# Kernel tuning notes

Hardware: AMD Instinct MI355X
Metric: run time of the kernel (lower is better)

Reference implementation:

```python
import jax, jax.numpy as jnp
import numpy as np

EMBED_DIM = 256
NUM_HEADS = 8
HEAD_DIM = EMBED_DIM // NUM_HEADS
SCALE = HEAD_DIM ** (-0.5)
L, B = 2048, 2


def setup_inputs() -> dict:
    key = jax.random.key(0)
    ks = jax.random.split(key, 12)
    s = EMBED_DIM ** (-0.5)
    return {
        "query": jax.random.normal(ks[0], (L, B, EMBED_DIM), jnp.float32),
        "key_": jax.random.normal(ks[1], (L, B, EMBED_DIM), jnp.float32),
        "value": jax.random.normal(ks[2], (L, B, EMBED_DIM), jnp.float32),
        "Wq": jax.random.normal(ks[3], (EMBED_DIM, EMBED_DIM), jnp.float32) * s,
        "bq": jnp.zeros((EMBED_DIM,), jnp.float32),
        "Wk": jax.random.normal(ks[4], (EMBED_DIM, EMBED_DIM), jnp.float32) * s,
        "bk": jnp.zeros((EMBED_DIM,), jnp.float32),
        "Wv": jax.random.normal(ks[5], (EMBED_DIM, EMBED_DIM), jnp.float32) * s,
        "bv": jnp.zeros((EMBED_DIM,), jnp.float32),
        "Wp": jax.random.normal(ks[6], (EMBED_DIM, EMBED_DIM), jnp.float32) * s,
        "bp": jnp.zeros((EMBED_DIM,), jnp.float32),
    }


def reference(query, key_, value, Wq, bq, Wk, bk, Wv, bv, Wp, bp):
    # Inputs are seq-first: [L, B, E]. Dropout treated as eval (identity).
    Lq, Bq, E = query.shape
    q = (query @ Wq + bq).reshape(Lq, Bq, NUM_HEADS, HEAD_DIM)
    k = (key_ @ Wk + bk).reshape(key_.shape[0], Bq, NUM_HEADS, HEAD_DIM)
    v = (value @ Wv + bv).reshape(value.shape[0], Bq, NUM_HEADS, HEAD_DIM)
    # scores: [B, H, Lq, Lk]
    attn = jnp.einsum('qbhd,kbhd->bhqk', q, k) * SCALE
    attn = jax.nn.softmax(attn, axis=-1)
    out = jnp.einsum('bhqk,kbhd->qbhd', attn, v).reshape(Lq, Bq, E)
    return out @ Wp + bp
```

## Files before the change

### kernel.cpp

```cpp
#include <hip/hip_runtime.h>
#include <math.h>

#define L_SEQ 2048
#define BATCH 2
#define EMB   256
#define NH    8
#define HD    32
#define NROW  (L_SEQ * BATCH)
#define SCALE 0.17677669529663687f
#define LOG2E 1.4426950408889634f
#define SCLAMP 60.0f

typedef __attribute__((ext_vector_type(8))) short          short8;
typedef __attribute__((ext_vector_type(8))) unsigned short ushort8v;
typedef __attribute__((ext_vector_type(4))) unsigned short ushort4v;
typedef __attribute__((ext_vector_type(4))) float          floatx4;

__device__ __forceinline__ unsigned short f2b(float x) {
    unsigned int u = __float_as_uint(x);
    unsigned int r = u + 0x7FFFu + ((u >> 16) & 1u);
    return (unsigned short)(r >> 16);
}

__device__ __forceinline__ unsigned int pack2bf(float lo, float hi) {
    unsigned int ulo = __float_as_uint(lo);
    unsigned int uhi = __float_as_uint(hi);
    ulo += 0x7FFFu + ((ulo >> 16) & 1u);
    uhi += 0x7FFFu + ((uhi >> 16) & 1u);
    return __builtin_amdgcn_perm(uhi, ulo, 0x07060302);
}

__device__ __forceinline__ float b2f(unsigned short u) {
    return __uint_as_float(((unsigned int)u) << 16);
}

__device__ __forceinline__ float hw_exp2(float x) {
    return __builtin_amdgcn_exp2f(x);
}

__global__ __launch_bounds__(256) void wtrans_kernel(const float* __restrict__ Wq,
                                                     const float* __restrict__ Wk,
                                                     const float* __restrict__ Wv,
                                                     const float* __restrict__ Wp,
                                                     unsigned short* __restrict__ out) {
    __shared__ unsigned short T[64][65];
    const int wsel = blockIdx.z;
    const float* W = (wsel == 0) ? Wq : (wsel == 1) ? Wk : (wsel == 2) ? Wv : Wp;
    const float scale = (wsel == 0) ? (SCALE * LOG2E) : 1.0f;
    unsigned short* dst = out + (size_t)wsel * EMB * EMB;
    const int k0 = blockIdx.x * 64, n0 = blockIdx.y * 64;
    const int tid = threadIdx.x;

    #pragma unroll
    for (int i = 0; i < 4; ++i) {
        int idx = tid + 256 * i;
        int r = idx >> 4, c4 = (idx & 15) * 4;
        float4 f = *(const float4*)&W[(size_t)(k0 + r) * EMB + n0 + c4];
        T[r][c4 + 0] = f2b(f.x * scale);
        T[r][c4 + 1] = f2b(f.y * scale);
        T[r][c4 + 2] = f2b(f.z * scale);
        T[r][c4 + 3] = f2b(f.w * scale);
    }
    __syncthreads();
    #pragma unroll
    for (int i = 0; i < 4; ++i) {
        int idx = tid + 256 * i;
        int rn = idx >> 4, ck = (idx & 15) * 4;
        ushort4v p;
        #pragma unroll
        for (int j = 0; j < 4; ++j) p[j] = T[ck + j][rn];
        *(ushort4v*)&dst[(size_t)(n0 + rn) * EMB + k0 + ck] = p;
    }
}

__global__ __launch_bounds__(256) void qkv_proj(const float* __restrict__ Xq,
                                                const float* __restrict__ Xk,
                                                const float* __restrict__ Xv,
                                                const unsigned short* __restrict__ Wt,
                                                const float* __restrict__ bq,
                                                const float* __restrict__ bk,
                                                const float* __restrict__ bv,
                                                unsigned short* __restrict__ outq,
                                                unsigned short* __restrict__ outk,
                                                unsigned short* __restrict__ outvt) {
    __shared__ unsigned short Xs[64][136];
    __shared__ unsigned short Ws[64][136];
    const int z = blockIdx.z;
    const float* X    = (z == 0) ? Xq : (z == 1) ? Xk : Xv;
    const float* bias = (z == 0) ? bq : (z == 1) ? bk : bv;
    const float bscale = (z == 0) ? (SCALE * LOG2E) : 1.0f;
    const unsigned short* W = Wt + (size_t)z * EMB * EMB;

    const int row0 = blockIdx.x * 64;
    const int col0 = blockIdx.y * 64;
    const int tid  = threadIdx.x;
    const int w    = tid >> 6;
    const int lane = tid & 63;
    const int l16  = lane & 15;
    const int quad = lane >> 4;

    floatx4 acc[4];
    #pragma unroll
    for (int g = 0; g < 4; ++g) acc[g] = (floatx4){0.f, 0.f, 0.f, 0.f};

    #pragma unroll
    for (int kh = 0; kh < 2; ++kh) {
        if (kh) __syncthreads();
        #pragma unroll
        for (int i = 0; i < 4; ++i) {
            int idx = tid + 256 * i;
            int r = idx >> 4, c8 = (idx & 15) * 8;
            const float4* xp = (const float4*)&X[(size_t)(row0 + r) * EMB + kh * 128 + c8];
            float4 f0 = xp[0], f1 = xp[1];
            uint4 pk;
            pk.x = pack2bf(f0.x, f0.y); pk.y = pack2bf(f0.z, f0.w);
            pk.z = pack2bf(f1.x, f1.y); pk.w = pack2bf(f1.z, f1.w);
            *(uint4*)&Xs[r][c8] = pk;
            *(ushort8v*)&Ws[r][c8] =
                *(const ushort8v*)&W[(size_t)(col0 + r) * EMB + kh * 128 + c8];
        }
        __syncthreads();

        #pragma unroll
        for (int k = 0; k < 128; k += 32) {
            short8 a = *(const short8*)&Xs[w * 16 + l16][k + quad * 8];
            #pragma unroll
            for (int g = 0; g < 4; ++g) {
                short8 bf = *(const short8*)&Ws[g * 16 + l16][k + quad * 8];
                acc[g] = __builtin_amdgcn_mfma_f32_16x16x32_bf16(a, bf, acc[g], 0, 0, 0);
            }
        }
    }

    if (z == 2) {
        __syncthreads();
        #pragma unroll
        for (int g = 0; g < 4; ++g) {
            int n = g * 16 + l16;
            float bb = bias[col0 + n] * bscale;
            #pragma unroll
            for (int r = 0; r < 4; ++r)
                Xs[w * 16 + quad * 4 + r][n] = f2b(acc[g][r] + bb);
        }
        __syncthreads();
        #pragma unroll
        for (int i = 0; i < 2; ++i) {
            int idx = tid + 256 * i;
            int n = idx >> 3, sub = idx & 7;
            int bb2 = sub >> 2, lq = sub & 3;
            ushort8v p;
            #pragma unroll
            for (int j = 0; j < 8; ++j) p[j] = Xs[(lq * 8 + j) * 2 + bb2][n];
            int h = (col0 + n) >> 5, d = (col0 + n) & 31;
            size_t base = ((size_t)(bb2 * NH + h) * HD + d) * L_SEQ + (row0 >> 1) + lq * 8;
            *(ushort8v*)&outvt[base] = p;
        }
    } else {
        unsigned short* outp = z ? outk : outq;
        #pragma unroll
        for (int g = 0; g < 4; ++g) {
            int c = col0 + g * 16 + l16;
            float bb = bias[c] * bscale;
            #pragma unroll
            for (int r = 0; r < 4; ++r) {
                int rg = row0 + w * 16 + quad * 4 + r;
                int b = rg & 1, ll = rg >> 1;
                int h = c >> 5, d = c & 31;
                outp[(((size_t)(b * NH + h) * L_SEQ) + ll) * HD + d] = f2b(acc[g][r] + bb);
            }
        }
    }
}

__global__ __launch_bounds__(256) void attn_kernel(const unsigned short* __restrict__ Q,
                                                   const unsigned short* __restrict__ K,
                                                   const unsigned short* __restrict__ Vt,
                                                   unsigned short* __restrict__ Opart,
                                                   float* __restrict__ lpart) {
    __shared__ unsigned short Vs[2][32][136];
    __shared__ unsigned short Ps[4][16][136];

    const int tid  = threadIdx.x;
    const int w    = tid >> 6;
    const int lane = tid & 63;
    const int l16  = lane & 15;
    const int quad = lane >> 4;

    const int l0   = blockIdx.x * 64;
    const int h    = blockIdx.y;
    const int b    = blockIdx.z & 1;
    const int half = blockIdx.z >> 1;
    const int koff = half * (L_SEQ / 2);
    const size_t bh = (size_t)(b * NH + h);

    const unsigned short* Qg  = Q  + (bh * L_SEQ) * HD;
    const unsigned short* Kg  = K  + (bh * L_SEQ + koff) * HD;
    const unsigned short* Vtg = Vt + (bh * HD) * L_SEQ + koff;

    short8 qfrag = *(const short8*)&Qg[(size_t)(l0 + w * 16 + l16) * HD + quad * 8];

    float lacc = 0.0f;
    floatx4 o0 = {0.f, 0.f, 0.f, 0.f};
    floatx4 o1 = {0.f, 0.f, 0.f, 0.f};
    const floatx4 zero4 = {0.f, 0.f, 0.f, 0.f};

    const int vd = tid >> 3;
    const int vj = (tid & 7) * 8;

    short8 kf[8];
    #pragma unroll
    for (int g = 0; g < 8; ++g)
        kf[g] = *(const short8*)&Kg[(size_t)(g * 16 + l16) * HD + quad * 8];

    *(ushort8v*)&Vs[0][vd][vj]      = *(const ushort8v*)&Vtg[(size_t)vd * L_SEQ + vj];
    *(ushort8v*)&Vs[0][vd][64 + vj] = *(const ushort8v*)&Vtg[(size_t)vd * L_SEQ + 64 + vj];

    const int NT = (L_SEQ / 2) / 128;
    for (int kt = 0; kt < NT; ++kt) {
        __syncthreads();

        floatx4 s[8];
        #pragma unroll
        for (int g = 0; g < 8; ++g)
            s[g] = __builtin_amdgcn_mfma_f32_16x16x32_bf16(kf[g], qfrag, zero4, 0, 0, 0);

        ushort8v vn0, vn1;
        if (kt + 1 < NT) {
            #pragma unroll
            for (int g = 0; g < 8; ++g)
                kf[g] = *(const short8*)
                    &Kg[(size_t)((kt + 1) * 128 + g * 16 + l16) * HD + quad * 8];
            vn0 = *(const ushort8v*)&Vtg[(size_t)vd * L_SEQ + (kt + 1) * 128 + vj];
            vn1 = *(const ushort8v*)&Vtg[(size_t)vd * L_SEQ + (kt + 1) * 128 + 64 + vj];
        }

        #pragma unroll
        for (int g = 0; g < 8; ++g) {
            float p0 = hw_exp2(fminf(s[g][0], SCLAMP));
            float p1 = hw_exp2(fminf(s[g][1], SCLAMP));
            float p2 = hw_exp2(fminf(s[g][2], SCLAMP));
            float p3 = hw_exp2(fminf(s[g][3], SCLAMP));
            lacc += (p0 + p1) + (p2 + p3);
            uint2 pk;
            pk.x = pack2bf(p0, p1);
            pk.y = pack2bf(p2, p3);
            *(uint2*)&Ps[w][l16][g * 16 + quad * 4] = pk;
        }

        const unsigned short (*Vc)[136] = Vs[kt & 1];
        #pragma unroll
        for (int c = 0; c < 4; ++c) {
            short8 pf = *(const short8*)&Ps[w][l16][c * 32 + quad * 8];
            short8 va = *(const short8*)&Vc[l16][c * 32 + quad * 8];
            short8 vb = *(const short8*)&Vc[16 + l16][c * 32 + quad * 8];
            o0 = __builtin_amdgcn_mfma_f32_16x16x32_bf16(va, pf, o0, 0, 0, 0);
            o1 = __builtin_amdgcn_mfma_f32_16x16x32_bf16(vb, pf, o1, 0, 0, 0);
        }

        if (kt + 1 < NT) {
            *(ushort8v*)&Vs[(kt + 1) & 1][vd][vj]      = vn0;
            *(ushort8v*)&Vs[(kt + 1) & 1][vd][64 + vj] = vn1;
        }
    }

    lacc += __shfl_xor(lacc, 16);
    lacc += __shfl_xor(lacc, 32);

    int query = l0 + w * 16 + l16;
    if (lane < 16)
        lpart[(size_t)half * (BATCH * NH * L_SEQ) + bh * L_SEQ + query] = lacc;

    size_t base = (size_t)half * ((size_t)NROW * EMB) +
                  ((size_t)query * BATCH + b) * EMB + h * HD;
    uint2 e0, e1;
    e0.x = pack2bf(o0[0], o0[1]);
    e0.y = pack2bf(o0[2], o0[3]);
    e1.x = pack2bf(o1[0], o1[1]);
    e1.y = pack2bf(o1[2], o1[3]);
    *(uint2*)&Opart[base + quad * 4] = e0;
    *(uint2*)&Opart[base + 16 + quad * 4] = e1;
}

__global__ __launch_bounds__(256) void out_proj(const unsigned short* __restrict__ Opart,
                                                const float* __restrict__ lpart,
                                                const unsigned short* __restrict__ Wt,
                                                const float* __restrict__ bias,
                                                float* __restrict__ out) {
    __shared__ unsigned short Xs[32][264];
    __shared__ unsigned short Ws[32][264];
    const int row0 = blockIdx.x * 32;
    const int col0 = blockIdx.y * 32;
    const int tid  = threadIdx.x;
    const int w    = tid >> 6;
    const int rw   = (w & 1) * 16;
    const int cw   = (w >> 1) * 16;
    const int lane = tid & 63;
    const int l16  = lane & 15;
    const int quad = lane >> 4;

    const size_t OP = (size_t)NROW * EMB;
    const size_t LP = (size_t)BATCH * NH * L_SEQ;

    #pragma unroll
    for (int i = 0; i < 4; ++i) {
        int idx = tid + 256 * i;
        int r = idx >> 5, c8 = (idx & 31) * 8;
        int rg = row0 + r;
        int bb = rg & 1, q = rg >> 1, hh = c8 >> 5;
        size_t lidx = ((size_t)(bb * NH + hh)) * L_SEQ + q;
        float inv = __builtin_amdgcn_rcpf(lpart[lidx] + lpart[LP + lidx]);

        ushort8v u0 = *(const ushort8v*)&Opart[(size_t)rg * EMB + c8];
        ushort8v u1 = *(const ushort8v*)&Opart[OP + (size_t)rg * EMB + c8];
        uint4 pk;
        pk.x = pack2bf((b2f(u0[0]) + b2f(u1[0])) * inv, (b2f(u0[1]) + b2f(u1[1])) * inv);
        pk.y = pack2bf((b2f(u0[2]) + b2f(u1[2])) * inv, (b2f(u0[3]) + b2f(u1[3])) * inv);
        pk.z = pack2bf((b2f(u0[4]) + b2f(u1[4])) * inv, (b2f(u0[5]) + b2f(u1[5])) * inv);
        pk.w = pack2bf((b2f(u0[6]) + b2f(u1[6])) * inv, (b2f(u0[7]) + b2f(u1[7])) * inv);
        *(uint4*)&Xs[r][c8] = pk;

        *(ushort8v*)&Ws[r][c8] = *(const ushort8v*)&Wt[(size_t)(col0 + r) * EMB + c8];
    }
    __syncthreads();

    floatx4 acc = {0.f, 0.f, 0.f, 0.f};
    #pragma unroll
    for (int k = 0; k < EMB; k += 32) {
        short8 a  = *(const short8*)&Xs[rw + l16][k + quad * 8];
        short8 bf = *(const short8*)&Ws[cw + l16][k + quad * 8];
        acc = __builtin_amdgcn_mfma_f32_16x16x32_bf16(a, bf, acc, 0, 0, 0);
    }

    int c = col0 + cw + l16;
    float bb = bias[c];
    #pragma unroll
    for (int r = 0; r < 4; ++r) {
        int rg = row0 + rw + quad * 4 + r;
        out[(size_t)rg * EMB + c] = acc[r] + bb;
    }
}

extern "C" void kernel_launch(void* const* d_in, const int* in_sizes, int n_in,
                              void* d_out, int out_size, void* d_ws, size_t ws_size,
                              hipStream_t stream) {
    const float* query = (const float*)d_in[0];
    const float* key_  = (const float*)d_in[1];
    const float* value = (const float*)d_in[2];
    const float* Wq    = (const float*)d_in[3];
    const float* bq    = (const float*)d_in[4];
    const float* Wk    = (const float*)d_in[5];
    const float* bk    = (const float*)d_in[6];
    const float* Wv    = (const float*)d_in[7];
    const float* bv    = (const float*)d_in[8];
    const float* Wp    = (const float*)d_in[9];
    const float* bp    = (const float*)d_in[10];
    float* out = (float*)d_out;

    unsigned short* ws = (unsigned short*)d_ws;
    const size_t WSZ = (size_t)EMB * EMB;
    const size_t M   = (size_t)NROW * EMB;
    unsigned short* wt    = ws;
    unsigned short* qw    = ws + 4 * WSZ;
    unsigned short* kw    = qw + M;
    unsigned short* vtw   = kw + M;
    unsigned short* opart = vtw + M;
    float*          lpart = (float*)(opart + 2 * M);

    wtrans_kernel<<<dim3(4, 4, 4), 256, 0, stream>>>(Wq, Wk, Wv, Wp, wt);

    qkv_proj<<<dim3(NROW / 64, EMB / 64, 3), 256, 0, stream>>>(
        query, key_, value, wt, bq, bk, bv, qw, kw, vtw);

    attn_kernel<<<dim3(L_SEQ / 64, NH, BATCH * 2), 256, 0, stream>>>(
        qw, kw, vtw, opart, lpart);

    out_proj<<<dim3(NROW / 32, EMB / 32), 256, 0, stream>>>(
        opart, lpart, wt + 3 * WSZ, bp, out);
}
```

Before: 117.8 us.

## Fuse four-kernel pipeline into one cooperative persistent kernel with grid syncs

Replaces the four separate launches (weight transpose, QKV projection, attention, output projection) with a single cooperative kernel of 512 persistent blocks. The stages are separated by grid.sync and share LDS through a union. The goal is to remove per-launch overhead and inter-kernel gaps. The trade-offs are grid-wide barrier costs, a fixed 512-block grid that makes blocks loop over the 768 and 1024 work units, and occupancy limited by launch_bounds(256,2). If the cooperative launch fails, it falls back to the old four kernels.

```diff
diff --git a/kernel.cpp b/kernel.cpp
--- a/kernel.cpp
+++ b/kernel.cpp
@@ -1,5 +1,8 @@
 #include <hip/hip_runtime.h>
+#include <hip/hip_cooperative_groups.h>
 #include <math.h>
+
+namespace cg = cooperative_groups;
 
 #define L_SEQ 2048
 #define BATCH 2
@@ -36,6 +39,306 @@
 
 __device__ __forceinline__ float hw_exp2(float x) {
     return __builtin_amdgcn_exp2f(x);
+}
+
+union ShMem {
+    struct { unsigned short T[64][65]; } p0;
+    struct { unsigned short Xs[64][136]; unsigned short Ws[64][136]; } p1;
+    struct { unsigned short Vs[2][32][136]; unsigned short Ps[4][16][136]; } p2;
+    struct { unsigned short Xs[32][264]; unsigned short Ws[32][264]; } p3;
+};
+
+#define COOP_BLOCKS 512
+
+__global__ __launch_bounds__(256, 2) void fused_attention(
+    const float* __restrict__ Xq, const float* __restrict__ Xk,
+    const float* __restrict__ Xv,
+    const float* __restrict__ Wq, const float* __restrict__ bq_,
+    const float* __restrict__ Wk, const float* __restrict__ bk_,
+    const float* __restrict__ Wv, const float* __restrict__ bv_,
+    const float* __restrict__ Wp, const float* __restrict__ bp_,
+    float* __restrict__ out,
+    unsigned short* __restrict__ wt, unsigned short* __restrict__ qw,
+    unsigned short* __restrict__ kw, unsigned short* __restrict__ vtw,
+    unsigned short* __restrict__ opart, float* __restrict__ lpart) {
+    __shared__ ShMem sh;
+    cg::grid_group grid = cg::this_grid();
+
+    const int bid  = blockIdx.x;
+    const int tid  = threadIdx.x;
+    const int w    = tid >> 6;
+    const int lane = tid & 63;
+    const int l16  = lane & 15;
+    const int quad = lane >> 4;
+    const floatx4 zero4 = {0.f, 0.f, 0.f, 0.f};
+
+    if (bid < 64) {
+        const int wsel = bid >> 4;
+        const int k0   = ((bid >> 2) & 3) * 64;
+        const int n0   = (bid & 3) * 64;
+        const float* W = (wsel == 0) ? Wq : (wsel == 1) ? Wk : (wsel == 2) ? Wv : Wp;
+        const float scale = (wsel == 0) ? (SCALE * LOG2E) : 1.0f;
+        unsigned short* dst = wt + (size_t)wsel * EMB * EMB;
+
+        #pragma unroll
+        for (int i = 0; i < 4; ++i) {
+            int idx = tid + 256 * i;
+            int r = idx >> 4, c4 = (idx & 15) * 4;
+            float4 f = *(const float4*)&W[(size_t)(k0 + r) * EMB + n0 + c4];
+            sh.p0.T[r][c4 + 0] = f2b(f.x * scale);
+            sh.p0.T[r][c4 + 1] = f2b(f.y * scale);
+            sh.p0.T[r][c4 + 2] = f2b(f.z * scale);
+            sh.p0.T[r][c4 + 3] = f2b(f.w * scale);
+        }
+        __syncthreads();
+        #pragma unroll
+        for (int i = 0; i < 4; ++i) {
+            int idx = tid + 256 * i;
+            int rn = idx >> 4, ck = (idx & 15) * 4;
+            ushort4v p;
+            #pragma unroll
+            for (int j = 0; j < 4; ++j) p[j] = sh.p0.T[ck + j][rn];
+            *(ushort4v*)&dst[(size_t)(n0 + rn) * EMB + k0 + ck] = p;
+        }
+    }
+    grid.sync();
+
+    for (int u = bid; u < 768; u += COOP_BLOCKS) {
+        __syncthreads();
+        const int z    = u >> 8;
+        const int rem  = u & 255;
+        const int row0 = (rem & 63) * 64;
+        const int col0 = (rem >> 6) * 64;
+        const float* X    = (z == 0) ? Xq : (z == 1) ? Xk : Xv;
+        const float* bias = (z == 0) ? bq_ : (z == 1) ? bk_ : bv_;
+        const float bscale = (z == 0) ? (SCALE * LOG2E) : 1.0f;
+        const unsigned short* W = wt + (size_t)z * EMB * EMB;
+
+        floatx4 acc[4] = {zero4, zero4, zero4, zero4};
+
+        #pragma unroll
+        for (int kh = 0; kh < 2; ++kh) {
+            if (kh) __syncthreads();
+            #pragma unroll
+            for (int i = 0; i < 4; ++i) {
+                int idx = tid + 256 * i;
+                int r = idx >> 4, c8 = (idx & 15) * 8;
+                const float4* xp =
+                    (const float4*)&X[(size_t)(row0 + r) * EMB + kh * 128 + c8];
+                float4 f0 = xp[0], f1 = xp[1];
+                uint4 pk;
+                pk.x = pack2bf(f0.x, f0.y); pk.y = pack2bf(f0.z, f0.w);
+                pk.z = pack2bf(f1.x, f1.y); pk.w = pack2bf(f1.z, f1.w);
+                *(uint4*)&sh.p1.Xs[r][c8] = pk;
+                *(ushort8v*)&sh.p1.Ws[r][c8] =
+                    *(const ushort8v*)&W[(size_t)(col0 + r) * EMB + kh * 128 + c8];
+            }
+            __syncthreads();
+            #pragma unroll
+            for (int k = 0; k < 128; k += 32) {
+                short8 a = *(const short8*)&sh.p1.Xs[w * 16 + l16][k + quad * 8];
+                #pragma unroll
+                for (int g = 0; g < 4; ++g) {
+                    short8 bf = *(const short8*)&sh.p1.Ws[g * 16 + l16][k + quad * 8];
+                    acc[g] = __builtin_amdgcn_mfma_f32_16x16x32_bf16(a, bf, acc[g], 0, 0, 0);
+                }
+            }
+        }
+
+        if (z == 2) {
+            __syncthreads();
+            #pragma unroll
+            for (int g = 0; g < 4; ++g) {
+                int n = g * 16 + l16;
+                float bb = bias[col0 + n] * bscale;
+                #pragma unroll
+                for (int r = 0; r < 4; ++r)
+                    sh.p1.Xs[w * 16 + quad * 4 + r][n] = f2b(acc[g][r] + bb);
+            }
+            __syncthreads();
+            #pragma unroll
+            for (int i = 0; i < 2; ++i) {
+                int idx = tid + 256 * i;
+                int n = idx >> 3, sub = idx & 7;
+                int bb2 = sub >> 2, lq = sub & 3;
+                ushort8v p;
+                #pragma unroll
+                for (int j = 0; j < 8; ++j) p[j] = sh.p1.Xs[(lq * 8 + j) * 2 + bb2][n];
+                int h = (col0 + n) >> 5, d = (col0 + n) & 31;
+                size_t base = ((size_t)(bb2 * NH + h) * HD + d) * L_SEQ +
+                              (row0 >> 1) + lq * 8;
+                *(ushort8v*)&vtw[base] = p;
+            }
+        } else {
+            unsigned short* outp = z ? kw : qw;
+            #pragma unroll
+            for (int g = 0; g < 4; ++g) {
+                int c = col0 + g * 16 + l16;
+                float bb = bias[c] * bscale;
+                #pragma unroll
+                for (int r = 0; r < 4; ++r) {
+                    int rg = row0 + w * 16 + quad * 4 + r;
+                    int b = rg & 1, ll = rg >> 1;
+                    int h = c >> 5, d = c & 31;
+                    outp[(((size_t)(b * NH + h) * L_SEQ) + ll) * HD + d] =
+                        f2b(acc[g][r] + bb);
+                }
+            }
+        }
+    }
+    grid.sync();
+
+    for (int u = bid; u < 1024; u += COOP_BLOCKS) {
+        const int l0   = (u & 31) * 64;
+        const int h    = (u >> 5) & 7;
+        const int z2   = u >> 8;
+        const int b    = z2 & 1;
+        const int half = z2 >> 1;
+        const int koff = half * (L_SEQ / 2);
+        const size_t bh = (size_t)(b * NH + h);
+
+        const unsigned short* Qg  = qw  + (bh * L_SEQ) * HD;
+        const unsigned short* Kg  = kw  + (bh * L_SEQ + koff) * HD;
+        const unsigned short* Vtg = vtw + (bh * HD) * L_SEQ + koff;
+
+        short8 qfrag = *(const short8*)&Qg[(size_t)(l0 + w * 16 + l16) * HD + quad * 8];
+
+        float lacc = 0.0f;
+        floatx4 o0 = zero4, o1 = zero4;
+        const int vd = tid >> 3;
+        const int vj = (tid & 7) * 8;
+
+        short8 kf[8];
+        #pragma unroll
+        for (int g = 0; g < 8; ++g)
+            kf[g] = *(const short8*)&Kg[(size_t)(g * 16 + l16) * HD + quad * 8];
+
+        *(ushort8v*)&sh.p2.Vs[0][vd][vj] =
+            *(const ushort8v*)&Vtg[(size_t)vd * L_SEQ + vj];
+        *(ushort8v*)&sh.p2.Vs[0][vd][64 + vj] =
+            *(const ushort8v*)&Vtg[(size_t)vd * L_SEQ + 64 + vj];
+
+        const int NT = (L_SEQ / 2) / 128;
+        for (int kt = 0; kt < NT; ++kt) {
+            __syncthreads();
+
+            floatx4 s[8];
+            #pragma unroll
+            for (int g = 0; g < 8; ++g)
+                s[g] = __builtin_amdgcn_mfma_f32_16x16x32_bf16(kf[g], qfrag, zero4, 0, 0, 0);
+
+            ushort8v vn0, vn1;
+            if (kt + 1 < NT) {
+                #pragma unroll
+                for (int g = 0; g < 8; ++g)
+                    kf[g] = *(const short8*)
+                        &Kg[(size_t)((kt + 1) * 128 + g * 16 + l16) * HD + quad * 8];
+                vn0 = *(const ushort8v*)&Vtg[(size_t)vd * L_SEQ + (kt + 1) * 128 + vj];
+                vn1 = *(const ushort8v*)&Vtg[(size_t)vd * L_SEQ + (kt + 1) * 128 + 64 + vj];
+            }
+
+            #pragma unroll
+            for (int g = 0; g < 8; ++g) {
+                float p0 = hw_exp2(fminf(s[g][0], SCLAMP));
+                float p1 = hw_exp2(fminf(s[g][1], SCLAMP));
+                float p2 = hw_exp2(fminf(s[g][2], SCLAMP));
+                float p3 = hw_exp2(fminf(s[g][3], SCLAMP));
+                lacc += (p0 + p1) + (p2 + p3);
+                uint2 pk;
+                pk.x = pack2bf(p0, p1);
+                pk.y = pack2bf(p2, p3);
+                *(uint2*)&sh.p2.Ps[w][l16][g * 16 + quad * 4] = pk;
+            }
+
+            const unsigned short (*Vc)[136] = sh.p2.Vs[kt & 1];
+            #pragma unroll
+            for (int c = 0; c < 4; ++c) {
+                short8 pf = *(const short8*)&sh.p2.Ps[w][l16][c * 32 + quad * 8];
+                short8 va = *(const short8*)&Vc[l16][c * 32 + quad * 8];
+                short8 vb = *(const short8*)&Vc[16 + l16][c * 32 + quad * 8];
+                o0 = __builtin_amdgcn_mfma_f32_16x16x32_bf16(va, pf, o0, 0, 0, 0);
+                o1 = __builtin_amdgcn_mfma_f32_16x16x32_bf16(vb, pf, o1, 0, 0, 0);
+            }
+
+            if (kt + 1 < NT) {
+                *(ushort8v*)&sh.p2.Vs[(kt + 1) & 1][vd][vj]      = vn0;
+                *(ushort8v*)&sh.p2.Vs[(kt + 1) & 1][vd][64 + vj] = vn1;
+            }
+        }
+
+        lacc += __shfl_xor(lacc, 16);
+        lacc += __shfl_xor(lacc, 32);
+
+        int qidx = l0 + w * 16 + l16;
+        if (lane < 16)
+            lpart[(size_t)half * (BATCH * NH * L_SEQ) + bh * L_SEQ + qidx] = lacc;
+
+        size_t base = (size_t)half * ((size_t)NROW * EMB) +
+                      ((size_t)qidx * BATCH + b) * EMB + h * HD;
+        uint2 e0, e1;
+        e0.x = pack2bf(o0[0], o0[1]);
+        e0.y = pack2bf(o0[2], o0[3]);
+        e1.x = pack2bf(o1[0], o1[1]);
+        e1.y = pack2bf(o1[2], o1[3]);
+        *(uint2*)&opart[base + quad * 4] = e0;
+        *(uint2*)&opart[base + 16 + quad * 4] = e1;
+        __syncthreads();
+    }
+    grid.sync();
+
+    for (int u = bid; u < 1024; u += COOP_BLOCKS) {
+        __syncthreads();
+        const int row0 = (u & 127) * 32;
+        const int col0 = (u >> 7) * 32;
+        const int rw   = (w & 1) * 16;
+        const int cw   = (w >> 1) * 16;
+        const size_t OP = (size_t)NROW * EMB;
+        const size_t LP = (size_t)BATCH * NH * L_SEQ;
+
+        #pragma unroll
+        for (int i = 0; i < 4; ++i) {
+            int idx = tid + 256 * i;
+            int r = idx >> 5, c8 = (idx & 31) * 8;
+            int rg = row0 + r;
+            int bb = rg & 1, q = rg >> 1, hh = c8 >> 5;
+            size_t lidx = ((size_t)(bb * NH + hh)) * L_SEQ + q;
+            float inv = __builtin_amdgcn_rcpf(lpart[lidx] + lpart[LP + lidx]);
+
+            ushort8v u0 = *(const ushort8v*)&opart[(size_t)rg * EMB + c8];
+            ushort8v u1 = *(const ushort8v*)&opart[OP + (size_t)rg * EMB + c8];
+            uint4 pk;
+            pk.x = pack2bf((b2f(u0[0]) + b2f(u1[0])) * inv,
+                           (b2f(u0[1]) + b2f(u1[1])) * inv);
+            pk.y = pack2bf((b2f(u0[2]) + b2f(u1[2])) * inv,
+                           (b2f(u0[3]) + b2f(u1[3])) * inv);
+            pk.z = pack2bf((b2f(u0[4]) + b2f(u1[4])) * inv,
+                           (b2f(u0[5]) + b2f(u1[5])) * inv);
+            pk.w = pack2bf((b2f(u0[6]) + b2f(u1[6])) * inv,
+                           (b2f(u0[7]) + b2f(u1[7])) * inv);
+            *(uint4*)&sh.p3.Xs[r][c8] = pk;
+
+            *(ushort8v*)&sh.p3.Ws[r][c8] =
+                *(const ushort8v*)&wt[(size_t)3 * EMB * EMB +
+                                      (size_t)(col0 + r) * EMB + c8];
+        }
+        __syncthreads();
+
+        floatx4 acc = zero4;
+        #pragma unroll
+        for (int k = 0; k < EMB; k += 32) {
+            short8 a  = *(const short8*)&sh.p3.Xs[rw + l16][k + quad * 8];
+            short8 bf = *(const short8*)&sh.p3.Ws[cw + l16][k + quad * 8];
+            acc = __builtin_amdgcn_mfma_f32_16x16x32_bf16(a, bf, acc, 0, 0, 0);
+        }
+
+        int c = col0 + cw + l16;
+        float bb = bp_[c];
+        #pragma unroll
+        for (int r = 0; r < 4; ++r) {
+            int rg = row0 + rw + quad * 4 + r;
+            out[(size_t)rg * EMB + c] = acc[r] + bb;
+        }
+    }
 }
 
 __global__ __launch_bounds__(256) void wtrans_kernel(const float* __restrict__ Wq,
@@ -98,10 +401,9 @@
     const int lane = tid & 63;
     const int l16  = lane & 15;
     const int quad = lane >> 4;
-
-    floatx4 acc[4];
-    #pragma unroll
-    for (int g = 0; g < 4; ++g) acc[g] = (floatx4){0.f, 0.f, 0.f, 0.f};
+    const floatx4 zero4 = {0.f, 0.f, 0.f, 0.f};
+
+    floatx4 acc[4] = {zero4, zero4, zero4, zero4};
 
     #pragma unroll
     for (int kh = 0; kh < 2; ++kh) {
@@ -120,7 +422,6 @@
                 *(const ushort8v*)&W[(size_t)(col0 + r) * EMB + kh * 128 + c8];
         }
         __syncthreads();
-
         #pragma unroll
         for (int k = 0; k < 128; k += 32) {
             short8 a = *(const short8*)&Xs[w * 16 + l16][k + quad * 8];
@@ -200,9 +501,8 @@
     short8 qfrag = *(const short8*)&Qg[(size_t)(l0 + w * 16 + l16) * HD + quad * 8];
 
     float lacc = 0.0f;
-    floatx4 o0 = {0.f, 0.f, 0.f, 0.f};
-    floatx4 o1 = {0.f, 0.f, 0.f, 0.f};
     const floatx4 zero4 = {0.f, 0.f, 0.f, 0.f};
+    floatx4 o0 = zero4, o1 = zero4;
 
     const int vd = tid >> 3;
     const int vj = (tid & 7) * 8;
@@ -366,14 +666,24 @@
     unsigned short* opart = vtw + M;
     float*          lpart = (float*)(opart + 2 * M);
 
-    wtrans_kernel<<<dim3(4, 4, 4), 256, 0, stream>>>(Wq, Wk, Wv, Wp, wt);
-
-    qkv_proj<<<dim3(NROW / 64, EMB / 64, 3), 256, 0, stream>>>(
-        query, key_, value, wt, bq, bk, bv, qw, kw, vtw);
-
-    attn_kernel<<<dim3(L_SEQ / 64, NH, BATCH * 2), 256, 0, stream>>>(
-        qw, kw, vtw, opart, lpart);
-
-    out_proj<<<dim3(NROW / 32, EMB / 32), 256, 0, stream>>>(
-        opart, lpart, wt + 3 * WSZ, bp, out);
-}
+    void* args[] = {
+        (void*)&query, (void*)&key_, (void*)&value,
+        (void*)&Wq, (void*)&bq, (void*)&Wk, (void*)&bk,
+        (void*)&Wv, (void*)&bv, (void*)&Wp, (void*)&bp,
+        (void*)&out,
+        (void*)&wt, (void*)&qw, (void*)&kw, (void*)&vtw,
+        (void*)&opart, (void*)&lpart
+    };
+    hipError_t err = hipLaunchCooperativeKernel((void*)fused_attention,
+                                                dim3(COOP_BLOCKS), dim3(256),
+                                                args, 0, stream);
+    if (err != hipSuccess) {
+        wtrans_kernel<<<dim3(4, 4, 4), 256, 0, stream>>>(Wq, Wk, Wv, Wp, wt);
+        qkv_proj<<<dim3(NROW / 64, EMB / 64, 3), 256, 0, stream>>>(
+            query, key_, value, wt, bq, bk, bv, qw, kw, vtw);
+        attn_kernel<<<dim3(L_SEQ / 64, NH, BATCH * 2), 256, 0, stream>>>(
+            qw, kw, vtw, opart, lpart);
+        out_proj<<<dim3(NROW / 32, EMB / 32), 256, 0, stream>>>(
+            opart, lpart, wt + 3 * WSZ, bp, out);
+    }
+}
```

New measurement: 309.0 us. +162.3%, slower.

## Fuse weight transpose into projections and read V fragments directly from global

Applied to the files above, without the earlier changes.

Drops the separate weight-transpose kernel. The QKV and output projection kernels now load fp32 weights, convert them to bf16 and transpose them into shared memory themselves, which removes one launch and one workspace round trip. The attention kernel also drops its double-buffered V tile in shared memory and the per-iteration barrier, loading V fragments straight from global into registers instead. The costs are repeated weight conversion in every block, scattered 2-byte shared-memory stores that may cause bank conflicts, and more global and L2 traffic for V.

```diff
diff --git a/kernel.cpp b/kernel.cpp
--- a/kernel.cpp
+++ b/kernel.cpp
@@ -13,7 +13,6 @@
 
 typedef __attribute__((ext_vector_type(8))) short          short8;
 typedef __attribute__((ext_vector_type(8))) unsigned short ushort8v;
-typedef __attribute__((ext_vector_type(4))) unsigned short ushort4v;
 typedef __attribute__((ext_vector_type(4))) float          floatx4;
 
 __device__ __forceinline__ unsigned short f2b(float x) {
@@ -38,45 +37,12 @@
     return __builtin_amdgcn_exp2f(x);
 }
 
-__global__ __launch_bounds__(256) void wtrans_kernel(const float* __restrict__ Wq,
-                                                     const float* __restrict__ Wk,
-                                                     const float* __restrict__ Wv,
-                                                     const float* __restrict__ Wp,
-                                                     unsigned short* __restrict__ out) {
-    __shared__ unsigned short T[64][65];
-    const int wsel = blockIdx.z;
-    const float* W = (wsel == 0) ? Wq : (wsel == 1) ? Wk : (wsel == 2) ? Wv : Wp;
-    const float scale = (wsel == 0) ? (SCALE * LOG2E) : 1.0f;
-    unsigned short* dst = out + (size_t)wsel * EMB * EMB;
-    const int k0 = blockIdx.x * 64, n0 = blockIdx.y * 64;
-    const int tid = threadIdx.x;
-
-    #pragma unroll
-    for (int i = 0; i < 4; ++i) {
-        int idx = tid + 256 * i;
-        int r = idx >> 4, c4 = (idx & 15) * 4;
-        float4 f = *(const float4*)&W[(size_t)(k0 + r) * EMB + n0 + c4];
-        T[r][c4 + 0] = f2b(f.x * scale);
-        T[r][c4 + 1] = f2b(f.y * scale);
-        T[r][c4 + 2] = f2b(f.z * scale);
-        T[r][c4 + 3] = f2b(f.w * scale);
-    }
-    __syncthreads();
-    #pragma unroll
-    for (int i = 0; i < 4; ++i) {
-        int idx = tid + 256 * i;
-        int rn = idx >> 4, ck = (idx & 15) * 4;
-        ushort4v p;
-        #pragma unroll
-        for (int j = 0; j < 4; ++j) p[j] = T[ck + j][rn];
-        *(ushort4v*)&dst[(size_t)(n0 + rn) * EMB + k0 + ck] = p;
-    }
-}
-
 __global__ __launch_bounds__(256) void qkv_proj(const float* __restrict__ Xq,
                                                 const float* __restrict__ Xk,
                                                 const float* __restrict__ Xv,
-                                                const unsigned short* __restrict__ Wt,
+                                                const float* __restrict__ Wqf,
+                                                const float* __restrict__ Wkf,
+                                                const float* __restrict__ Wvf,
                                                 const float* __restrict__ bq,
                                                 const float* __restrict__ bk,
                                                 const float* __restrict__ bv,
@@ -87,9 +53,9 @@
     __shared__ unsigned short Ws[64][136];
     const int z = blockIdx.z;
     const float* X    = (z == 0) ? Xq : (z == 1) ? Xk : Xv;
+    const float* Wf   = (z == 0) ? Wqf : (z == 1) ? Wkf : Wvf;
     const float* bias = (z == 0) ? bq : (z == 1) ? bk : bv;
-    const float bscale = (z == 0) ? (SCALE * LOG2E) : 1.0f;
-    const unsigned short* W = Wt + (size_t)z * EMB * EMB;
+    const float wscale = (z == 0) ? (SCALE * LOG2E) : 1.0f;
 
     const int row0 = blockIdx.x * 64;
     const int col0 = blockIdx.y * 64;
@@ -98,10 +64,9 @@
     const int lane = tid & 63;
     const int l16  = lane & 15;
     const int quad = lane >> 4;
-
-    floatx4 acc[4];
-    #pragma unroll
-    for (int g = 0; g < 4; ++g) acc[g] = (floatx4){0.f, 0.f, 0.f, 0.f};
+    const floatx4 zero4 = {0.f, 0.f, 0.f, 0.f};
+
+    floatx4 acc[4] = {zero4, zero4, zero4, zero4};
 
     #pragma unroll
     for (int kh = 0; kh < 2; ++kh) {
@@ -110,14 +75,24 @@
         for (int i = 0; i < 4; ++i) {
             int idx = tid + 256 * i;
             int r = idx >> 4, c8 = (idx & 15) * 8;
-            const float4* xp = (const float4*)&X[(size_t)(row0 + r) * EMB + kh * 128 + c8];
+            const float4* xp =
+                (const float4*)&X[(size_t)(row0 + r) * EMB + kh * 128 + c8];
             float4 f0 = xp[0], f1 = xp[1];
             uint4 pk;
             pk.x = pack2bf(f0.x, f0.y); pk.y = pack2bf(f0.z, f0.w);
             pk.z = pack2bf(f1.x, f1.y); pk.w = pack2bf(f1.z, f1.w);
             *(uint4*)&Xs[r][c8] = pk;
-            *(ushort8v*)&Ws[r][c8] =
-                *(const ushort8v*)&W[(size_t)(col0 + r) * EMB + kh * 128 + c8];
+        }
+        #pragma unroll
+        for (int i = 0; i < 8; ++i) {
+            int idx = tid + 256 * i;
+            int k  = idx >> 4;
+            int n4 = (idx & 15) * 4;
+            float4 f = *(const float4*)&Wf[(size_t)(kh * 128 + k) * EMB + col0 + n4];
+            Ws[n4 + 0][k] = f2b(f.x * wscale);
+            Ws[n4 + 1][k] = f2b(f.y * wscale);
+            Ws[n4 + 2][k] = f2b(f.z * wscale);
+            Ws[n4 + 3][k] = f2b(f.w * wscale);
         }
         __syncthreads();
 
@@ -137,7 +112,7 @@
         #pragma unroll
         for (int g = 0; g < 4; ++g) {
             int n = g * 16 + l16;
-            float bb = bias[col0 + n] * bscale;
+            float bb = bias[col0 + n];
             #pragma unroll
             for (int r = 0; r < 4; ++r)
                 Xs[w * 16 + quad * 4 + r][n] = f2b(acc[g][r] + bb);
@@ -157,6 +132,7 @@
         }
     } else {
         unsigned short* outp = z ? outk : outq;
+        const float bscale = (z == 0) ? (SCALE * LOG2E) : 1.0f;
         #pragma unroll
         for (int g = 0; g < 4; ++g) {
             int c = col0 + g * 16 + l16;
@@ -177,7 +153,6 @@
                                                    const unsigned short* __restrict__ Vt,
                                                    unsigned short* __restrict__ Opart,
                                                    float* __restrict__ lpart) {
-    __shared__ unsigned short Vs[2][32][136];
     __shared__ unsigned short Ps[4][16][136];
 
     const int tid  = threadIdx.x;
@@ -200,38 +175,35 @@
     short8 qfrag = *(const short8*)&Qg[(size_t)(l0 + w * 16 + l16) * HD + quad * 8];
 
     float lacc = 0.0f;
-    floatx4 o0 = {0.f, 0.f, 0.f, 0.f};
-    floatx4 o1 = {0.f, 0.f, 0.f, 0.f};
     const floatx4 zero4 = {0.f, 0.f, 0.f, 0.f};
-
-    const int vd = tid >> 3;
-    const int vj = (tid & 7) * 8;
+    floatx4 o0 = zero4, o1 = zero4;
 
     short8 kf[8];
     #pragma unroll
     for (int g = 0; g < 8; ++g)
         kf[g] = *(const short8*)&Kg[(size_t)(g * 16 + l16) * HD + quad * 8];
 
-    *(ushort8v*)&Vs[0][vd][vj]      = *(const ushort8v*)&Vtg[(size_t)vd * L_SEQ + vj];
-    *(ushort8v*)&Vs[0][vd][64 + vj] = *(const ushort8v*)&Vtg[(size_t)vd * L_SEQ + 64 + vj];
-
     const int NT = (L_SEQ / 2) / 128;
     for (int kt = 0; kt < NT; ++kt) {
-        __syncthreads();
+        short8 vf0[4], vf1[4];
+        #pragma unroll
+        for (int c = 0; c < 4; ++c) {
+            vf0[c] = *(const short8*)
+                &Vtg[(size_t)l16 * L_SEQ + kt * 128 + c * 32 + quad * 8];
+            vf1[c] = *(const short8*)
+                &Vtg[(size_t)(16 + l16) * L_SEQ + kt * 128 + c * 32 + quad * 8];
+        }
 
         floatx4 s[8];
         #pragma unroll
         for (int g = 0; g < 8; ++g)
             s[g] = __builtin_amdgcn_mfma_f32_16x16x32_bf16(kf[g], qfrag, zero4, 0, 0, 0);
 
-        ushort8v vn0, vn1;
         if (kt + 1 < NT) {
             #pragma unroll
             for (int g = 0; g < 8; ++g)
                 kf[g] = *(const short8*)
                     &Kg[(size_t)((kt + 1) * 128 + g * 16 + l16) * HD + quad * 8];
-            vn0 = *(const ushort8v*)&Vtg[(size_t)vd * L_SEQ + (kt + 1) * 128 + vj];
-            vn1 = *(const ushort8v*)&Vtg[(size_t)vd * L_SEQ + (kt + 1) * 128 + 64 + vj];
         }
 
         #pragma unroll
@@ -247,19 +219,11 @@
             *(uint2*)&Ps[w][l16][g * 16 + quad * 4] = pk;
         }
 
-        const unsigned short (*Vc)[136] = Vs[kt & 1];
         #pragma unroll
         for (int c = 0; c < 4; ++c) {
             short8 pf = *(const short8*)&Ps[w][l16][c * 32 + quad * 8];
-            short8 va = *(const short8*)&Vc[l16][c * 32 + quad * 8];
-            short8 vb = *(const short8*)&Vc[16 + l16][c * 32 + quad * 8];
-            o0 = __builtin_amdgcn_mfma_f32_16x16x32_bf16(va, pf, o0, 0, 0, 0);
-            o1 = __builtin_amdgcn_mfma_f32_16x16x32_bf16(vb, pf, o1, 0, 0, 0);
-        }
-
-        if (kt + 1 < NT) {
-            *(ushort8v*)&Vs[(kt + 1) & 1][vd][vj]      = vn0;
-            *(ushort8v*)&Vs[(kt + 1) & 1][vd][64 + vj] = vn1;
+            o0 = __builtin_amdgcn_mfma_f32_16x16x32_bf16(vf0[c], pf, o0, 0, 0, 0);
+            o1 = __builtin_amdgcn_mfma_f32_16x16x32_bf16(vf1[c], pf, o1, 0, 0, 0);
         }
     }
 
@@ -283,7 +247,7 @@
 
 __global__ __launch_bounds__(256) void out_proj(const unsigned short* __restrict__ Opart,
                                                 const float* __restrict__ lpart,
-                                                const unsigned short* __restrict__ Wt,
+                                                const float* __restrict__ Wpf,
                                                 const float* __restrict__ bias,
                                                 float* __restrict__ out) {
     __shared__ unsigned short Xs[32][264];
@@ -318,8 +282,17 @@
         pk.z = pack2bf((b2f(u0[4]) + b2f(u1[4])) * inv, (b2f(u0[5]) + b2f(u1[5])) * inv);
         pk.w = pack2bf((b2f(u0[6]) + b2f(u1[6])) * inv, (b2f(u0[7]) + b2f(u1[7])) * inv);
         *(uint4*)&Xs[r][c8] = pk;
-
-        *(ushort8v*)&Ws[r][c8] = *(const ushort8v*)&Wt[(size_t)(col0 + r) * EMB + c8];
+    }
+    #pragma unroll
+    for (int i = 0; i < 8; ++i) {
+        int idx = tid + 256 * i;
+        int k  = idx >> 3;
+        int n4 = (idx & 7) * 4;
+        float4 f = *(const float4*)&Wpf[(size_t)k * EMB + col0 + n4];
+        Ws[n4 + 0][k] = f2b(f.x);
+        Ws[n4 + 1][k] = f2b(f.y);
+        Ws[n4 + 2][k] = f2b(f.z);
+        Ws[n4 + 3][k] = f2b(f.w);
     }
     __syncthreads();
 
@@ -357,23 +330,19 @@
     float* out = (float*)d_out;
 
     unsigned short* ws = (unsigned short*)d_ws;
-    const size_t WSZ = (size_t)EMB * EMB;
-    const size_t M   = (size_t)NROW * EMB;
-    unsigned short* wt    = ws;
-    unsigned short* qw    = ws + 4 * WSZ;
+    const size_t M = (size_t)NROW * EMB;
+    unsigned short* qw    = ws;
     unsigned short* kw    = qw + M;
     unsigned short* vtw   = kw + M;
     unsigned short* opart = vtw + M;
     float*          lpart = (float*)(opart + 2 * M);
 
-    wtrans_kernel<<<dim3(4, 4, 4), 256, 0, stream>>>(Wq, Wk, Wv, Wp, wt);
-
     qkv_proj<<<dim3(NROW / 64, EMB / 64, 3), 256, 0, stream>>>(
-        query, key_, value, wt, bq, bk, bv, qw, kw, vtw);
+        query, key_, value, Wq, Wk, Wv, bq, bk, bv, qw, kw, vtw);
 
     attn_kernel<<<dim3(L_SEQ / 64, NH, BATCH * 2), 256, 0, stream>>>(
         qw, kw, vtw, opart, lpart);
 
-    out_proj<<<dim3(NROW / 32, EMB / 32), 256, 0, stream>>>(
-        opart, lpart, wt + 3 * WSZ, bp, out);
-}
+    out_proj<<<dim3(NROW / 32, EMB / 8 / 4), 256, 0, stream>>>(
+        opart, lpart, Wp, bp, out);
+}
```

Measured after the change: 140.5 us. 1.19x slower.
